# Kernel tuning notes

Hardware: AMD Instinct MI355X
Metric: run time of the kernel (lower is better)

## Reference

```python
import jax, jax.numpy as jnp
import numpy as np
import math

N_HEAD = 8
KERNEL_EPS = 1e-3   # performer-pytorch kernel_epsilon
BN_EPS = 1e-5


def _orthogonal_random_features(m, d, seed=0):
    # gaussian_orthogonal_random_matrix with scaling=0 (performer-pytorch)
    rng = np.random.default_rng(seed)
    blocks = []
    for _ in range(math.ceil(m / d)):
        q, _ = np.linalg.qr(rng.standard_normal((d, d)))
        blocks.append(q.T)
    final = np.concatenate(blocks, axis=0)[:m]
    multiplier = np.linalg.norm(rng.standard_normal((m, d)), axis=1)
    return (multiplier[:, None] * final).astype(np.float32)


def setup_inputs() -> dict:
    key = jax.random.key(0)
    ks = jax.random.split(key, 12)
    B, C, H, W = 16, 256, 56, 56
    d_head = C // N_HEAD                       # 32
    m = int(d_head * math.log(d_head))         # 110 (nb_features default)
    s = 0.02
    inp = {
        "x": jax.random.normal(ks[0], (B, C, H, W), jnp.float32),
        "bn1_gamma": jnp.ones((C,), jnp.float32),
        "bn1_beta": jnp.zeros((C,), jnp.float32),
        "bn2_gamma": jnp.ones((C,), jnp.float32),
        "bn2_beta": jnp.zeros((C,), jnp.float32),
        "Wq": jax.random.normal(ks[1], (C, C), jnp.float32) * s,
        "bq": jnp.zeros((C,), jnp.float32),
        "Wk": jax.random.normal(ks[2], (C, C), jnp.float32) * s,
        "bk": jnp.zeros((C,), jnp.float32),
        "Wv": jax.random.normal(ks[3], (C, C), jnp.float32) * s,
        "bv": jnp.zeros((C,), jnp.float32),
        "Wo": jax.random.normal(ks[4], (C, C), jnp.float32) * s,
        "bo": jnp.zeros((C,), jnp.float32),
        "proj": jnp.asarray(_orthogonal_random_features(m, d_head)),
        "conv_w": jax.random.normal(ks[5], (C, C, 3, 3), jnp.float32) * 0.02,
    }
    return inp


def _batchnorm(x, gamma, beta):
    # training-mode BatchNorm2d: batch statistics over (N, H, W)
    mean = jnp.mean(x, axis=(0, 2, 3), keepdims=True)
    var = jnp.var(x, axis=(0, 2, 3), keepdims=True)
    xn = (x - mean) * jax.lax.rsqrt(var + BN_EPS)
    return gamma[None, :, None, None] * xn + beta[None, :, None, None]


def _performer_attention(x, Wq, bq, Wk, bk, Wv, bv, Wo, bo, proj):
    # x: [B, C, H, W]; flatten spatial dims into a token sequence
    b, c, hh, ww = x.shape
    n = hh * ww
    d = c // N_HEAD
    t = x.reshape(b, c, n).transpose(0, 2, 1)  # [b, n, c]

    def split_heads(z):
        return z.reshape(b, n, N_HEAD, d).transpose(0, 2, 1, 3)  # [b, h, n, d]

    q = split_heads(t @ Wq + bq)
    k = split_heads(t @ Wk + bk)
    v = split_heads(t @ Wv + bv)

    # generalized (ReLU) kernel features, data_normalizer = d**-0.25
    norm = d ** -0.25
    phi_q = jax.nn.relu(jnp.einsum('bhnd,md->bhnm', q * norm, proj)) + KERNEL_EPS
    phi_k = jax.nn.relu(jnp.einsum('bhnd,md->bhnm', k * norm, proj)) + KERNEL_EPS

    # non-causal linear attention: O(n * m * d)
    k_sum = phi_k.sum(axis=2)                                   # [b, h, m]
    d_inv = 1.0 / jnp.einsum('bhnm,bhm->bhn', phi_q, k_sum)     # [b, h, n]
    ctx = jnp.einsum('bhnm,bhnd->bhmd', phi_k, v)               # [b, h, m, d]
    out = jnp.einsum('bhnm,bhmd->bhnd', phi_q, ctx) * d_inv[..., None]

    out = out.transpose(0, 2, 1, 3).reshape(b, n, c)            # merge heads
    out = out @ Wo + bo                                         # to_out (dropout = identity at eval)
    return out.transpose(0, 2, 1).reshape(b, c, hh, ww)


def reference(x, bn1_gamma, bn1_beta, bn2_gamma, bn2_beta,
              Wq, bq, Wk, bk, Wv, bv, Wo, bo, proj, conv_w):
    residual = x
    out = jax.nn.relu(_batchnorm(x, bn1_gamma, bn1_beta))
    out = _performer_attention(out, Wq, bq, Wk, bk, Wv, bv, Wo, bo, proj)
    out = out + x
    out = jax.nn.relu(_batchnorm(out, bn2_gamma, bn2_beta))
    out = jax.lax.conv_general_dilated(
        out, conv_w, window_strides=(1, 1), padding=((1, 1), (1, 1)),
        dimension_numbers=('NCHW', 'OIHW', 'NCHW'))
    return out + residual
```

## Files before the change

kernel.cpp:

```cpp
#include <hip/hip_runtime.h>


typedef short short8 __attribute__((ext_vector_type(8)));
typedef float f32x4 __attribute__((ext_vector_type(4)));

#define DEVI static __device__ __forceinline__

#define CDIM 256
#define SDIM 3136
#define NTOK 50176
#define NHEAD 8
#define DHEAD 32
#define MFEAT 110
#define NORMC 0.42044820762685725f
#define NPIX 50176.0f

DEVI unsigned short f2bf(float f) {
  union { float f; unsigned u; } v; v.f = f;
  unsigned r = v.u + 0x7fffu + ((v.u >> 16) & 1u);
  return (unsigned short)(r >> 16);
}

DEVI float bf2f(short h) {
  union { unsigned u; float f; } v;
  v.u = ((unsigned)(unsigned short)h) << 16;
  return v.f;
}

DEVI f32x4 mfma16(short8 a, short8 b, f32x4 c) {
  return __builtin_amdgcn_mfma_f32_16x16x32_bf16(a, b, c, 0, 0, 0);
}

DEVI unsigned long long pack4(const unsigned short* h) {
  return (unsigned long long)(h[0] | ((unsigned)h[1] << 16)) |
         ((unsigned long long)(h[2] | ((unsigned)h[3] << 16)) << 32);
}

__global__ void zero_kernel(float* p, int n) {
  for (int i = blockIdx.x * blockDim.x + threadIdx.x; i < n; i += gridDim.x * blockDim.x)
    p[i] = 0.f;
}

__global__ void prep_kernel(const float* __restrict__ Wq, const float* __restrict__ Wk,
                            const float* __restrict__ Wv, const float* __restrict__ Wo,
                            const float* __restrict__ proj, const float* __restrict__ conv_w,
                            short* __restrict__ Bqkv, short* __restrict__ WoT,
                            short* __restrict__ Bconv, short* __restrict__ projb) {
  const int t0 = blockIdx.x * blockDim.x + threadIdx.x;
  const int stride = gridDim.x * blockDim.x;
  for (int idx = t0; idx < 3 * 65536; idx += stride) {
    const int sel = idx >> 16, r = idx & 65535;
    const int ks = r >> 13, nf = (r >> 9) & 15, lane = (r >> 3) & 63, j = r & 7;
    const int n = nf * 16 + (lane & 15), k = ks * 32 + (lane >> 4) * 8 + j;
    const float* W = (sel == 0) ? Wq : ((sel == 1) ? Wk : Wv);
    Bqkv[idx] = (short)f2bf(W[k * 256 + n]);
  }
  for (int idx = t0; idx < 65536; idx += stride) {
    const int ks = idx >> 13, nf = (idx >> 9) & 15, lane = (idx >> 3) & 63, j = idx & 7;
    const int n = nf * 16 + (lane & 15), k = ks * 32 + (lane >> 4) * 8 + j;
    WoT[idx] = (short)f2bf(Wo[k * 256 + n]);
  }
  for (int idx = t0; idx < 9 * 65536; idx += stride) {
    const int off = idx >> 16, r = idx & 65535;
    const int ks = r >> 13, nf = (r >> 9) & 15, lane = (r >> 3) & 63, j = r & 7;
    const int oc = nf * 16 + (lane & 15), cin = ks * 32 + (lane >> 4) * 8 + j;
    Bconv[idx] = (short)f2bf(conv_w[(oc * 256 + cin) * 9 + off]);
  }
  for (int idx = t0; idx < 128 * 32; idx += stride) {
    const int row = idx >> 5, kk = idx & 31;
    const float v = (row < MFEAT) ? proj[row * 32 + kk] * NORMC : 0.f;
    projb[idx] = (short)f2bf(v);
  }
}

__global__ void bn_stats_kernel(const float* __restrict__ src, float* __restrict__ sums) {
  const int c = blockIdx.x & 255, b = blockIdx.x >> 8;
  const float* p = src + ((size_t)b * CDIM + c) * SDIM;
  float s = 0.f, s2 = 0.f;
  for (int i = threadIdx.x; i < SDIM; i += 256) {
    const float v = p[i];
    s += v; s2 += v * v;
  }
  for (int o = 32; o > 0; o >>= 1) { s += __shfl_down(s, o); s2 += __shfl_down(s2, o); }
  __shared__ float ls[4], ls2[4];
  const int w = threadIdx.x >> 6;
  if ((threadIdx.x & 63) == 0) { ls[w] = s; ls2[w] = s2; }
  __syncthreads();
  if (threadIdx.x == 0) {
    s = ls[0] + ls[1] + ls[2] + ls[3];
    s2 = ls2[0] + ls2[1] + ls2[2] + ls2[3];
    atomicAdd(&sums[c], s);
    atomicAdd(&sums[256 + c], s2);
  }
}

__global__ void bn_final_kernel(const float* __restrict__ sums, const float* __restrict__ gamma,
                                const float* __restrict__ beta, float* __restrict__ scsh) {
  const int c = threadIdx.x;
  const float mean = sums[c] * (1.f / NPIX);
  const float var = sums[256 + c] * (1.f / NPIX) - mean * mean;
  const float sc = gamma[c] * rsqrtf(var + 1e-5f);
  scsh[c] = sc;
  scsh[256 + c] = beta[c] - mean * sc;
}

__global__ void transpose_x(const float* __restrict__ x, const float* __restrict__ scsh,
                            short* __restrict__ dst, int mode) {
  __shared__ short T[64][72];
  const int t0 = blockIdx.x * 64;
  const int b = t0 / SDIM;
  const int s0 = t0 - b * SDIM;
  const int c0 = blockIdx.y * 64;
  const int tid = threadIdx.x;
  const int tokl = tid & 63, cl = tid >> 6;
  const float* xb = x + ((size_t)b * CDIM + c0) * SDIM + s0;
#pragma unroll
  for (int i = 0; i < 16; ++i) {
    const int c = i * 4 + cl;
    float v = xb[(size_t)c * SDIM + tokl];
    if (mode) v = fmaxf(v * scsh[c0 + c] + scsh[256 + c0 + c], 0.f);
    T[c][tokl] = (short)f2bf(v);
  }
  __syncthreads();
#pragma unroll
  for (int j = 0; j < 2; ++j) {
    const int idx = tid + j * 256;
    const int tk = idx >> 3, ch8 = idx & 7;
    unsigned short h[8];
#pragma unroll
    for (int jj = 0; jj < 8; ++jj) h[jj] = (unsigned short)T[ch8 * 8 + jj][tk];
    unsigned long long* p = (unsigned long long*)&dst[(size_t)(t0 + tk) * 256 + c0 + ch8 * 8];
    p[0] = pack4(h);
    p[1] = pack4(h + 4);
  }
}

__global__ __launch_bounds__(256, 4)
void qkv_gemm(const short* __restrict__ u1, const short* __restrict__ BT,
              const float* __restrict__ bq, const float* __restrict__ bk,
              const float* __restrict__ bv,
              short* __restrict__ qo, short* __restrict__ ko, short* __restrict__ vo) {
  __shared__ short A_s[64 * 256];
  const int tid = threadIdx.x;
  const int mtile = blockIdx.x, sel = blockIdx.y;
  const int token0 = mtile * 64;
  {
    const int trow = tid >> 5, cch = tid & 31;
    const short* src = u1 + (size_t)token0 * 256;
#pragma unroll
    for (int i = 0; i < 8; ++i) {
      const int tok = trow + i * 8;
      const short8 vv = *(const short8*)&src[tok * 256 + cch * 8];
      const int phys = cch ^ (tok & 31);
      *(short8*)&A_s[tok * 256 + phys * 8] = vv;
    }
  }
  __syncthreads();

  const int lane = tid & 63, wv = tid >> 6;
  const int quad = lane >> 4, l15 = lane & 15;
  const f32x4 vzero = {0.f, 0.f, 0.f, 0.f};
  f32x4 acc[4][4];
#pragma unroll
  for (int i = 0; i < 4; ++i)
#pragma unroll
    for (int j = 0; j < 4; ++j) acc[i][j] = vzero;
  const short* Bp = BT + ((size_t)sel << 16);
#pragma unroll
  for (int ks = 0; ks < 8; ++ks) {
    short8 af[4], bfr[4];
#pragma unroll
    for (int rf = 0; rf < 4; ++rf) {
      const int row = rf * 16 + l15;
      const int phys = (ks * 4 + quad) ^ (row & 31);
      af[rf] = *(const short8*)&A_s[row * 256 + phys * 8];
    }
#pragma unroll
    for (int cf = 0; cf < 4; ++cf)
      bfr[cf] = *(const short8*)&Bp[((((ks << 4) | (wv << 2) | cf) << 6) | lane) << 3];
#pragma unroll
    for (int rf = 0; rf < 4; ++rf)
#pragma unroll
      for (int cf = 0; cf < 4; ++cf)
        acc[rf][cf] = mfma16(af[rf], bfr[cf], acc[rf][cf]);
  }

  const int bb = token0 / SDIM;
  const int s0 = token0 - bb * SDIM;
#pragma unroll
  for (int cf = 0; cf < 4; ++cf) {
    const int chn = wv * 64 + cf * 16 + l15;
    const int head = chn >> 5, dd = chn & 31;
    const float bias = (sel == 0) ? bq[chn] : ((sel == 1) ? bk[chn] : bv[chn]);
#pragma unroll
    for (int rf = 0; rf < 4; ++rf) {
      const int ss = s0 + rf * 16 + quad * 4;
      if (sel < 2) {
        short* dst = (sel == 0) ? qo : ko;
        short* p = dst + ((size_t)(bb * NHEAD + head) * SDIM) * DHEAD + dd;
#pragma unroll
        for (int r = 0; r < 4; ++r)
          p[(size_t)(ss + r) * DHEAD] = (short)f2bf(acc[rf][cf][r] + bias);
      } else {
        unsigned short h4[4];
#pragma unroll
        for (int r = 0; r < 4; ++r) h4[r] = f2bf(acc[rf][cf][r] + bias);
        *(unsigned long long*)(vo + ((size_t)(bb * NHEAD + head) * DHEAD + dd) * SDIM + ss) = pack4(h4);
      }
    }
  }
}

__global__ __launch_bounds__(256, 2)
void attn_phase1(const short* __restrict__ kk, const short* __restrict__ vt,
                 const short* __restrict__ projb, float* __restrict__ ctx_acc,
                 float* __restrict__ ksum) {
  __shared__ short proj_s[128 * 40];
  __shared__ short phi_s[4][128 * 40];
  const int tid = threadIdx.x;
  const int bh = blockIdx.x >> 1, halfI = blockIdx.x & 1;
  for (int i = tid; i < 128 * 32; i += 256)
    proj_s[(i >> 5) * 40 + (i & 31)] = projb[i];
  __syncthreads();
  const int lane = tid & 63, wv = tid >> 6;
  const int quad = lane >> 4, l15 = lane & 15;
  const short* kb = kk + (size_t)bh * SDIM * DHEAD;
  const short* vb = vt + (size_t)bh * DHEAD * SDIM;
  short* myphi = phi_s[wv];
  const f32x4 vzero = {0.f, 0.f, 0.f, 0.f};
  f32x4 cacc[8][2];
  float ks_acc[8];
#pragma unroll
  for (int i = 0; i < 8; ++i) { cacc[i][0] = vzero; cacc[i][1] = vzero; ks_acc[i] = 0.f; }

  for (int ch = halfI * 4 + wv; ch < 98; ch += 8) {
    const int tok0 = ch * 32;
    short8 afr[2];
    afr[0] = *(const short8*)&kb[(size_t)(tok0 + l15) * DHEAD + quad * 8];
    afr[1] = *(const short8*)&kb[(size_t)(tok0 + 16 + l15) * DHEAD + quad * 8];
#pragma unroll
    for (int cf = 0; cf < 8; ++cf) {
      const short8 bfr = *(const short8*)&proj_s[(cf * 16 + l15) * 40 + quad * 8];
      const float epsv = (cf < 6) ? 1e-3f : ((cf == 6) ? ((l15 < 14) ? 1e-3f : 0.f) : 0.f);
#pragma unroll
      for (int fr = 0; fr < 2; ++fr) {
        f32x4 p = mfma16(afr[fr], bfr, vzero);
        unsigned short h4[4];
        float srow = 0.f;
#pragma unroll
        for (int r = 0; r < 4; ++r) {
          const float pv = fmaxf(p[r], 0.f) + epsv;
          srow += pv;
          h4[r] = f2bf(pv);
        }
        ks_acc[cf] += srow;
        *(unsigned long long*)&myphi[(cf * 16 + l15) * 40 + fr * 16 + quad * 4] = pack4(h4);
      }
    }
    short8 bv2[2];
    bv2[0] = *(const short8*)&vb[(size_t)l15 * SDIM + tok0 + quad * 8];
    bv2[1] = *(const short8*)&vb[(size_t)(16 + l15) * SDIM + tok0 + quad * 8];
#pragma unroll
    for (int mfr = 0; mfr < 8; ++mfr) {
      const short8 a2 = *(const short8*)&myphi[(mfr * 16 + l15) * 40 + quad * 8];
      cacc[mfr][0] = mfma16(a2, bv2[0], cacc[mfr][0]);
      cacc[mfr][1] = mfma16(a2, bv2[1], cacc[mfr][1]);
    }
  }
#pragma unroll
  for (int cf = 0; cf < 8; ++cf) {
    float v = ks_acc[cf];
    v += __shfl_xor(v, 16);
    v += __shfl_xor(v, 32);
    if (lane < 16) atomicAdd(&ksum[bh * 128 + cf * 16 + lane], v);
  }
  float* cb = ctx_acc + (size_t)bh * 4096;
#pragma unroll
  for (int mfr = 0; mfr < 8; ++mfr)
#pragma unroll
    for (int df = 0; df < 2; ++df)
#pragma unroll
      for (int r = 0; r < 4; ++r)
        atomicAdd(&cb[(mfr * 16 + quad * 4 + r) * 32 + df * 16 + l15], cacc[mfr][df][r]);
}

__global__ __launch_bounds__(256, 2)
void attn_phase2(const short* __restrict__ qq, const float* __restrict__ ctx_acc,
                 const float* __restrict__ ksum, const short* __restrict__ projb,
                 short* __restrict__ Yn) {
  __shared__ short proj_s[128 * 40];
  __shared__ short ctx_s[48 * 136];
  __shared__ short phi_s[4][32 * 136];
  const int tid = threadIdx.x;
  const int bh = blockIdx.x >> 1, halfI = blockIdx.x & 1;
  for (int i = tid; i < 128 * 32; i += 256)
    proj_s[(i >> 5) * 40 + (i & 31)] = projb[i];
  {
    const float* ca = ctx_acc + (size_t)bh * 4096;
    const float* ks = ksum + bh * 128;
    for (int i = tid; i < 48 * 128; i += 256) {
      const int row = i >> 7, mf = i & 127;
      const float v = (row < 32) ? ca[mf * 32 + row] : ((row == 32) ? ks[mf] : 0.f);
      ctx_s[row * 136 + mf] = (short)f2bf(v);
    }
  }
  __syncthreads();
  const int lane = tid & 63, wv = tid >> 6;
  const int quad = lane >> 4, l15 = lane & 15;
  const int b = bh >> 3, head = bh & 7;
  const short* qb = qq + (size_t)bh * SDIM * DHEAD;
  short* myphi = phi_s[wv];
  const f32x4 vzero = {0.f, 0.f, 0.f, 0.f};

  for (int ch = halfI * 4 + wv; ch < 98; ch += 8) {
    const int tok0 = ch * 32;
    short8 afr[2];
    afr[0] = *(const short8*)&qb[(size_t)(tok0 + l15) * DHEAD + quad * 8];
    afr[1] = *(const short8*)&qb[(size_t)(tok0 + 16 + l15) * DHEAD + quad * 8];
#pragma unroll
    for (int cf = 0; cf < 8; ++cf) {
      const short8 bfr = *(const short8*)&proj_s[(cf * 16 + l15) * 40 + quad * 8];
      const float epsv = (cf < 6) ? 1e-3f : ((cf == 6) ? ((l15 < 14) ? 1e-3f : 0.f) : 0.f);
#pragma unroll
      for (int fr = 0; fr < 2; ++fr) {
        f32x4 p = mfma16(afr[fr], bfr, vzero);
#pragma unroll
        for (int r = 0; r < 4; ++r) {
          const float pv = fmaxf(p[r], 0.f) + epsv;
          myphi[(fr * 16 + quad * 4 + r) * 136 + cf * 16 + l15] = (short)f2bf(pv);
        }
      }
    }
    f32x4 oacc[2][3];
#pragma unroll
    for (int fr = 0; fr < 2; ++fr)
#pragma unroll
      for (int c3 = 0; c3 < 3; ++c3) oacc[fr][c3] = vzero;
#pragma unroll
    for (int ksI = 0; ksI < 4; ++ksI) {
      short8 a3[2];
      a3[0] = *(const short8*)&myphi[l15 * 136 + ksI * 32 + quad * 8];
      a3[1] = *(const short8*)&myphi[(16 + l15) * 136 + ksI * 32 + quad * 8];
#pragma unroll
      for (int c3 = 0; c3 < 3; ++c3) {
        const short8 b3 = *(const short8*)&ctx_s[(c3 * 16 + l15) * 136 + ksI * 32 + quad * 8];
        oacc[0][c3] = mfma16(a3[0], b3, oacc[0][c3]);
        oacc[1][c3] = mfma16(a3[1], b3, oacc[1][c3]);
      }
    }
#pragma unroll
    for (int fr = 0; fr < 2; ++fr) {
      float dinv[4];
#pragma unroll
      for (int r = 0; r < 4; ++r) {
        const float den = __shfl(oacc[fr][2][r], quad << 4);
        dinv[r] = 1.f / den;
      }
#pragma unroll
      for (int c3 = 0; c3 < 2; ++c3)
#pragma unroll
        for (int r = 0; r < 4; ++r)
          myphi[(fr * 16 + quad * 4 + r) * 40 + c3 * 16 + l15] =
              (short)f2bf(oacc[fr][c3][r] * dinv[r]);
    }
    const size_t trow0 = (size_t)(b * SDIM + tok0) * 256 + head * 32;
#pragma unroll
    for (int it = 0; it < 2; ++it) {
      const int idx = it * 64 + lane;
      const int tl = idx >> 2, c4 = idx & 3;
      const short8 vv = *(const short8*)&myphi[tl * 40 + c4 * 8];
      *(short8*)&Yn[trow0 + (size_t)tl * 256 + c4 * 8] = vv;
    }
  }
}

__global__ __launch_bounds__(256, 4)
void wo_gemm(const short* __restrict__ Yn, const short* __restrict__ WoT,
             const float* __restrict__ bo, const short* __restrict__ xh,
             short* __restrict__ z, float* __restrict__ sums) {
  __shared__ short A_s[64 * 264];
  const int tid = threadIdx.x;
  const int mtile = blockIdx.x;
  const int token0 = mtile * 64;
  {
    const int trow = tid >> 5, cch = tid & 31;
    const short* src = Yn + (size_t)token0 * 256;
#pragma unroll
    for (int i = 0; i < 8; ++i) {
      const int tok = trow + i * 8;
      const short8 vv = *(const short8*)&src[tok * 256 + cch * 8];
      const int phys = cch ^ (tok & 31);
      *(short8*)&A_s[tok * 256 + phys * 8] = vv;
    }
  }
  __syncthreads();

  const int lane = tid & 63, wv = tid >> 6;
  const int quad = lane >> 4, l15 = lane & 15;
  const f32x4 vzero = {0.f, 0.f, 0.f, 0.f};
  f32x4 acc[4][4];
#pragma unroll
  for (int i = 0; i < 4; ++i)
#pragma unroll
    for (int j = 0; j < 4; ++j) acc[i][j] = vzero;
#pragma unroll
  for (int ks = 0; ks < 8; ++ks) {
    short8 af[4], bfr[4];
#pragma unroll
    for (int rf = 0; rf < 4; ++rf) {
      const int row = rf * 16 + l15;
      const int phys = (ks * 4 + quad) ^ (row & 31);
      af[rf] = *(const short8*)&A_s[row * 256 + phys * 8];
    }
#pragma unroll
    for (int cf = 0; cf < 4; ++cf)
      bfr[cf] = *(const short8*)&WoT[((((ks << 4) | (wv << 2) | cf) << 6) | lane) << 3];
#pragma unroll
    for (int rf = 0; rf < 4; ++rf)
#pragma unroll
      for (int cf = 0; cf < 4; ++cf)
        acc[rf][cf] = mfma16(af[rf], bfr[cf], acc[rf][cf]);
  }
  __syncthreads();
  short* zt = A_s;
#pragma unroll
  for (int cf = 0; cf < 4; ++cf) {
    const int ocl = wv * 64 + cf * 16 + l15;
    const float bias = bo[ocl];
#pragma unroll
    for (int rf = 0; rf < 4; ++rf) {
      const int tl = rf * 16 + quad * 4;
#pragma unroll
      for (int r = 0; r < 4; ++r)
        zt[(tl + r) * 264 + ocl] = (short)f2bf(acc[rf][cf][r] + bias);
    }
  }
  __syncthreads();
  float s[8], s2[8];
#pragma unroll
  for (int j = 0; j < 8; ++j) { s[j] = 0.f; s2[j] = 0.f; }
#pragma unroll
  for (int j = 0; j < 8; ++j) {
    const int idx = tid + j * 256;
    const int tl = idx >> 5, ch = idx & 31;
    const short8 zv = *(const short8*)&zt[tl * 264 + ch * 8];
    const size_t gbase = (size_t)(token0 + tl) * 256 + ch * 8;
    const short8 xv = *(const short8*)&xh[gbase];
    unsigned short h[8];
#pragma unroll
    for (int jj = 0; jj < 8; ++jj) {
      h[jj] = f2bf(bf2f(zv[jj]) + bf2f(xv[jj]));
      const float f = bf2f((short)h[jj]);
      s[jj] += f; s2[jj] += f * f;
    }
    unsigned long long* p = (unsigned long long*)&z[gbase];
    p[0] = pack4(h);
    p[1] = pack4(h + 4);
  }
  __syncthreads();
  float* L = (float*)A_s;
#pragma unroll
  for (int j = 0; j < 8; ++j) { L[tid * 16 + j] = s[j]; L[tid * 16 + 8 + j] = s2[j]; }
  __syncthreads();
  const int c = tid, cgi = c >> 3, j2 = c & 7;
  float a = 0.f, b2 = 0.f;
#pragma unroll
  for (int tr = 0; tr < 8; ++tr) {
    a += L[(tr * 32 + cgi) * 16 + j2];
    b2 += L[(tr * 32 + cgi) * 16 + 8 + j2];
  }
  atomicAdd(&sums[c], a);
  atomicAdd(&sums[256 + c], b2);
}

__global__ __launch_bounds__(256, 4)
void conv_gemm(const short* __restrict__ zin, const float* __restrict__ scsh,
               const short* __restrict__ Bc, const float* __restrict__ x,
               float* __restrict__ out) {
  __shared__ short A_s[40 * 256];
  const int tid = threadIdx.x;
  const int bid = blockIdx.x;
  const int mtile = (bid & 7) * 196 + (bid >> 3);
  const int bb = mtile / 98, s0 = (mtile - bb * 98) * 32;
  const short* ub = zin + (size_t)bb * SDIM * 256;
  const int lane = tid & 63, wv = tid >> 6;
  const int quad = lane >> 4, l15 = lane & 15;
  const f32x4 vzero = {0.f, 0.f, 0.f, 0.f};
  const short8 szero = {0, 0, 0, 0, 0, 0, 0, 0};
  f32x4 acc[2][4];
#pragma unroll
  for (int i = 0; i < 2; ++i)
#pragma unroll
    for (int j = 0; j < 4; ++j) acc[i][j] = vzero;

  const int cch = tid & 31;
  float sc_r[8], sh_r[8];
#pragma unroll
  for (int j = 0; j < 8; ++j) {
    sc_r[j] = scsh[cch * 8 + j];
    sh_r[j] = scsh[256 + cch * 8 + j];
  }

  int vy[2], vx[2];
#pragma unroll
  for (int rf = 0; rf < 2; ++rf) {
    const int so = s0 + rf * 16 + l15;
    vy[rf] = so / 56;
    vx[rf] = so - vy[rf] * 56;
  }

  short8 pref[5];
#define LOAD_DY(DYI)                                                           \
  {                                                                            \
    const int srow0 = s0 + ((DYI)-1) * 56 - 1;                                 \
    _Pragma("unroll") for (int it = 0; it < 5; ++it) {                         \
      const int chunk = tid + it * 256;                                        \
      const int idx = chunk >> 5;                                              \
      const int s = srow0 + idx;                                               \
      short8 vv = {0, 0, 0, 0, 0, 0, 0, 0};                                    \
      if ((unsigned)s < (unsigned)SDIM) {                                      \
        const short8 raw = *(const short8*)&ub[(size_t)s * 256 + cch * 8];     \
        unsigned short hh[8];                                                  \
        _Pragma("unroll") for (int jj = 0; jj < 8; ++jj)                       \
            hh[jj] = f2bf(fmaxf(bf2f(raw[jj]) * sc_r[jj] + sh_r[jj], 0.f));    \
        _Pragma("unroll") for (int jj = 0; jj < 8; ++jj)                       \
            vv[jj] = (short)hh[jj];                                            \
      }                                                                        \
      pref[it] = vv;                                                           \
    }                                                                          \
  }

  LOAD_DY(0);
#pragma unroll
  for (int dyi = 0; dyi < 3; ++dyi) {
    if (dyi) __syncthreads();
#pragma unroll
    for (int it = 0; it < 5; ++it) {
      const int chunk = tid + it * 256;
      const int idx = chunk >> 5;
      const int phys = cch ^ (idx & 31);
      *(short8*)&A_s[idx * 256 + phys * 8] = pref[it];
    }
    __syncthreads();
    if (dyi < 2) LOAD_DY(dyi + 1);
#pragma unroll
    for (int dxi = 0; dxi < 3; ++dxi) {
      const short* Bp = Bc + ((dyi * 3 + dxi) << 16);
      bool vmask[2];
#pragma unroll
      for (int rf = 0; rf < 2; ++rf)
        vmask[rf] = ((unsigned)(vy[rf] + dyi - 1) < 56u) &&
                    ((unsigned)(vx[rf] + dxi - 1) < 56u);
#pragma unroll
      for (int ks = 0; ks < 8; ++ks) {
        short8 af[2], bfr[4];
#pragma unroll
        for (int rf = 0; rf < 2; ++rf) {
          const int row = rf * 16 + l15 + dxi;
          const int phys = (ks * 4 + quad) ^ (row & 31);
          const short8 a = *(const short8*)&A_s[row * 256 + phys * 8];
          af[rf] = vmask[rf] ? a : szero;
        }
#pragma unroll
        for (int cf = 0; cf < 4; ++cf)
          bfr[cf] = *(const short8*)&Bp[((((ks << 4) | (wv << 2) | cf) << 6) | lane) << 3];
#pragma unroll
        for (int rf = 0; rf < 2; ++rf)
#pragma unroll
          for (int cf = 0; cf < 4; ++cf)
            acc[rf][cf] = mfma16(af[rf], bfr[cf], acc[rf][cf]);
      }
    }
  }
#undef LOAD_DY

#pragma unroll
  for (int cf = 0; cf < 4; ++cf) {
    const int oc = wv * 64 + cf * 16 + l15;
#pragma unroll
    for (int rf = 0; rf < 2; ++rf) {
      const int ss = s0 + rf * 16 + quad * 4;
      const size_t base = ((size_t)(bb * CDIM + oc)) * SDIM + ss;
      const f32x4 xv = *(const f32x4*)(x + base);
      f32x4 res;
#pragma unroll
      for (int r = 0; r < 4; ++r) res[r] = acc[rf][cf][r] + xv[r];
      *(f32x4*)(out + base) = res;
    }
  }
}

extern "C" void kernel_launch(void* const* d_in, const int* in_sizes, int n_in,
                              void* d_out, int out_size, void* d_ws, size_t ws_size,
                              hipStream_t stream) {
  const float* x      = (const float*)d_in[0];
  const float* bn1_g  = (const float*)d_in[1];
  const float* bn1_b  = (const float*)d_in[2];
  const float* bn2_g  = (const float*)d_in[3];
  const float* bn2_b  = (const float*)d_in[4];
  const float* Wq     = (const float*)d_in[5];
  const float* bq     = (const float*)d_in[6];
  const float* Wk     = (const float*)d_in[7];
  const float* bk     = (const float*)d_in[8];
  const float* Wv     = (const float*)d_in[9];
  const float* bv     = (const float*)d_in[10];
  const float* Wo     = (const float*)d_in[11];
  const float* bo     = (const float*)d_in[12];
  const float* proj   = (const float*)d_in[13];
  const float* conv_w = (const float*)d_in[14];
  float* out = (float*)d_out;
  char* ws = (char*)d_ws;

  const size_t OFF_K     = 0;
  const size_t OFF_V     = 25690112;
  const size_t OFF_BQKV  = 51380224;
  const size_t OFF_WOT   = 51773440;
  const size_t OFF_BCONV = 51904512;
  const size_t OFF_PROJB = 53084160;
  const size_t OFF_CTXA  = 53092352;
  const size_t OFF_KSUM  = 55189504;
  const size_t OFF_BN1S  = 55255040;
  const size_t OFF_BN2S  = 55257088;
  const size_t OFF_SC1   = 55259136;
  const size_t OFF_SC2   = 55261184;
  const size_t WS_NEEDED = 56836096;

  if (ws_size < WS_NEEDED) {
    zero_kernel<<<2048, 256, 0, stream>>>(out, out_size);
    return;
  }

  short* qb    = (short*)d_out;
  short* half2 = (short*)d_out + 12845056;
  short* kb    = (short*)(ws + OFF_K);
  short* vtb   = (short*)(ws + OFF_V);
  short* Yn    = (short*)(ws + OFF_K);
  short* zbuf  = (short*)(ws + OFF_V);
  short* Bqkv  = (short*)(ws + OFF_BQKV);
  short* WoT   = (short*)(ws + OFF_WOT);
  short* Bconv = (short*)(ws + OFF_BCONV);
  short* projb = (short*)(ws + OFF_PROJB);
  float* ctxa  = (float*)(ws + OFF_CTXA);
  float* ksum  = (float*)(ws + OFF_KSUM);
  float* bn1s  = (float*)(ws + OFF_BN1S);
  float* bn2s  = (float*)(ws + OFF_BN2S);
  float* sc1   = (float*)(ws + OFF_SC1);
  float* sc2   = (float*)(ws + OFF_SC2);

  zero_kernel<<<512, 256, 0, stream>>>(ctxa, (2097152 + 65536 + 2048 + 2048) / 4);
  prep_kernel<<<256, 256, 0, stream>>>(Wq, Wk, Wv, Wo, proj, conv_w, Bqkv, WoT, Bconv, projb);
  bn_stats_kernel<<<4096, 256, 0, stream>>>(x, bn1s);
  bn_final_kernel<<<1, 256, 0, stream>>>(bn1s, bn1_g, bn1_b, sc1);
  transpose_x<<<dim3(784, 4), 256, 0, stream>>>(x, sc1, half2, 1);
  qkv_gemm<<<dim3(784, 3), 256, 0, stream>>>(half2, Bqkv, bq, bk, bv, qb, kb, vtb);
  attn_phase1<<<256, 256, 0, stream>>>(kb, vtb, projb, ctxa, ksum);
  attn_phase2<<<256, 256, 0, stream>>>(qb, ctxa, ksum, projb, Yn);
  transpose_x<<<dim3(784, 4), 256, 0, stream>>>(x, sc1, half2, 0);
  wo_gemm<<<784, 256, 0, stream>>>(Yn, WoT, bo, half2, zbuf, bn2s);
  bn_final_kernel<<<1, 256, 0, stream>>>(bn2s, bn2_g, bn2_b, sc2);
  conv_gemm<<<1568, 256, 0, stream>>>(zbuf, sc2, Bconv, x, out);
}
```

Measured before the change: 516.6 us.

## Fuse residual into Wo epilogue, merge QKV passes, precompute BN2-ReLU tensor

The second transpose of x is removed: the Wo GEMM epilogue now reads fp32 x directly and adds the residual before rounding to bf16. The QKV GEMM loops over the three weight matrices inside one block, so the A tile is staged once instead of three times. BN2 plus ReLU is moved out of the conv prefetch into a separate elementwise kernel that writes a normalized bf16 buffer. This removes the ninefold redundant normalization in conv_gemm at the cost of an extra full-tensor read and write. attn_phase1 launch bounds are also raised to 3 blocks per CU.

Result: slower. 839.2 us (+62.4%).

```diff
diff --git a/kernel.cpp b/kernel.cpp
--- a/kernel.cpp
+++ b/kernel.cpp
@@ -105,7 +105,7 @@
 }
 
 __global__ void transpose_x(const float* __restrict__ x, const float* __restrict__ scsh,
-                            short* __restrict__ dst, int mode) {
+                            short* __restrict__ dst) {
   __shared__ short T[64][72];
   const int t0 = blockIdx.x * 64;
   const int b = t0 / SDIM;
@@ -118,7 +118,7 @@
   for (int i = 0; i < 16; ++i) {
     const int c = i * 4 + cl;
     float v = xb[(size_t)c * SDIM + tokl];
-    if (mode) v = fmaxf(v * scsh[c0 + c] + scsh[256 + c0 + c], 0.f);
+    v = fmaxf(v * scsh[c0 + c] + scsh[256 + c0 + c], 0.f);
     T[c][tokl] = (short)f2bf(v);
   }
   __syncthreads();
@@ -130,6 +130,25 @@
 #pragma unroll
     for (int jj = 0; jj < 8; ++jj) h[jj] = (unsigned short)T[ch8 * 8 + jj][tk];
     unsigned long long* p = (unsigned long long*)&dst[(size_t)(t0 + tk) * 256 + c0 + ch8 * 8];
+    p[0] = pack4(h);
+    p[1] = pack4(h + 4);
+  }
+}
+
+__global__ void u2_kernel(const short* __restrict__ z, const float* __restrict__ scsh,
+                          short* __restrict__ u2) {
+  const int nchunks = NTOK * 32;
+  for (int idx = blockIdx.x * blockDim.x + threadIdx.x; idx < nchunks;
+       idx += gridDim.x * blockDim.x) {
+    const int cch = idx & 31;
+    const short8 v = *(const short8*)&z[(size_t)idx * 8];
+    unsigned short h[8];
+#pragma unroll
+    for (int j = 0; j < 8; ++j) {
+      const int c = cch * 8 + j;
+      h[j] = f2bf(fmaxf(bf2f(v[j]) * scsh[c] + scsh[256 + c], 0.f));
+    }
+    unsigned long long* p = (unsigned long long*)&u2[(size_t)idx * 8];
     p[0] = pack4(h);
     p[1] = pack4(h + 4);
   }
@@ -142,7 +161,7 @@
               short* __restrict__ qo, short* __restrict__ ko, short* __restrict__ vo) {
   __shared__ short A_s[64 * 256];
   const int tid = threadIdx.x;
-  const int mtile = blockIdx.x, sel = blockIdx.y;
+  const int mtile = blockIdx.x;
   const int token0 = mtile * 64;
   {
     const int trow = tid >> 5, cch = tid & 31;
@@ -160,58 +179,61 @@
   const int lane = tid & 63, wv = tid >> 6;
   const int quad = lane >> 4, l15 = lane & 15;
   const f32x4 vzero = {0.f, 0.f, 0.f, 0.f};
-  f32x4 acc[4][4];
-#pragma unroll
-  for (int i = 0; i < 4; ++i)
-#pragma unroll
-    for (int j = 0; j < 4; ++j) acc[i][j] = vzero;
-  const short* Bp = BT + ((size_t)sel << 16);
-#pragma unroll
-  for (int ks = 0; ks < 8; ++ks) {
-    short8 af[4], bfr[4];
-#pragma unroll
-    for (int rf = 0; rf < 4; ++rf) {
-      const int row = rf * 16 + l15;
-      const int phys = (ks * 4 + quad) ^ (row & 31);
-      af[rf] = *(const short8*)&A_s[row * 256 + phys * 8];
-    }
-#pragma unroll
-    for (int cf = 0; cf < 4; ++cf)
-      bfr[cf] = *(const short8*)&Bp[((((ks << 4) | (wv << 2) | cf) << 6) | lane) << 3];
-#pragma unroll
-    for (int rf = 0; rf < 4; ++rf)
-#pragma unroll
-      for (int cf = 0; cf < 4; ++cf)
-        acc[rf][cf] = mfma16(af[rf], bfr[cf], acc[rf][cf]);
-  }
-
   const int bb = token0 / SDIM;
   const int s0 = token0 - bb * SDIM;
-#pragma unroll
-  for (int cf = 0; cf < 4; ++cf) {
-    const int chn = wv * 64 + cf * 16 + l15;
-    const int head = chn >> 5, dd = chn & 31;
-    const float bias = (sel == 0) ? bq[chn] : ((sel == 1) ? bk[chn] : bv[chn]);
-#pragma unroll
-    for (int rf = 0; rf < 4; ++rf) {
-      const int ss = s0 + rf * 16 + quad * 4;
-      if (sel < 2) {
-        short* dst = (sel == 0) ? qo : ko;
-        short* p = dst + ((size_t)(bb * NHEAD + head) * SDIM) * DHEAD + dd;
-#pragma unroll
-        for (int r = 0; r < 4; ++r)
-          p[(size_t)(ss + r) * DHEAD] = (short)f2bf(acc[rf][cf][r] + bias);
-      } else {
-        unsigned short h4[4];
-#pragma unroll
-        for (int r = 0; r < 4; ++r) h4[r] = f2bf(acc[rf][cf][r] + bias);
-        *(unsigned long long*)(vo + ((size_t)(bb * NHEAD + head) * DHEAD + dd) * SDIM + ss) = pack4(h4);
+
+  for (int sel = 0; sel < 3; ++sel) {
+    f32x4 acc[4][4];
+#pragma unroll
+    for (int i = 0; i < 4; ++i)
+#pragma unroll
+      for (int j = 0; j < 4; ++j) acc[i][j] = vzero;
+    const short* Bp = BT + ((size_t)sel << 16);
+#pragma unroll
+    for (int ks = 0; ks < 8; ++ks) {
+      short8 af[4], bfr[4];
+#pragma unroll
+      for (int rf = 0; rf < 4; ++rf) {
+        const int row = rf * 16 + l15;
+        const int phys = (ks * 4 + quad) ^ (row & 31);
+        af[rf] = *(const short8*)&A_s[row * 256 + phys * 8];
       }
-    }
-  }
-}
-
-__global__ __launch_bounds__(256, 2)
+#pragma unroll
+      for (int cf = 0; cf < 4; ++cf)
+        bfr[cf] = *(const short8*)&Bp[((((ks << 4) | (wv << 2) | cf) << 6) | lane) << 3];
+#pragma unroll
+      for (int rf = 0; rf < 4; ++rf)
+#pragma unroll
+        for (int cf = 0; cf < 4; ++cf)
+          acc[rf][cf] = mfma16(af[rf], bfr[cf], acc[rf][cf]);
+    }
+
+#pragma unroll
+    for (int cf = 0; cf < 4; ++cf) {
+      const int chn = wv * 64 + cf * 16 + l15;
+      const int head = chn >> 5, dd = chn & 31;
+      const float bias = (sel == 0) ? bq[chn] : ((sel == 1) ? bk[chn] : bv[chn]);
+#pragma unroll
+      for (int rf = 0; rf < 4; ++rf) {
+        const int ss = s0 + rf * 16 + quad * 4;
+        if (sel < 2) {
+          short* dst = (sel == 0) ? qo : ko;
+          short* p = dst + ((size_t)(bb * NHEAD + head) * SDIM) * DHEAD + dd;
+#pragma unroll
+          for (int r = 0; r < 4; ++r)
+            p[(size_t)(ss + r) * DHEAD] = (short)f2bf(acc[rf][cf][r] + bias);
+        } else {
+          unsigned short h4[4];
+#pragma unroll
+          for (int r = 0; r < 4; ++r) h4[r] = f2bf(acc[rf][cf][r] + bias);
+          *(unsigned long long*)(vo + ((size_t)(bb * NHEAD + head) * DHEAD + dd) * SDIM + ss) = pack4(h4);
+        }
+      }
+    }
+  }
+}
+
+__global__ __launch_bounds__(256, 3)
 void attn_phase1(const short* __restrict__ kk, const short* __restrict__ vt,
                  const short* __restrict__ projb, float* __restrict__ ctx_acc,
                  float* __restrict__ ksum) {
@@ -376,7 +398,7 @@
 
 __global__ __launch_bounds__(256, 4)
 void wo_gemm(const short* __restrict__ Yn, const short* __restrict__ WoT,
-             const float* __restrict__ bo, const short* __restrict__ xh,
+             const float* __restrict__ bo, const float* __restrict__ x,
              short* __restrict__ z, float* __restrict__ sums) {
   __shared__ short A_s[64 * 264];
   const int tid = threadIdx.x;
@@ -421,6 +443,8 @@
       for (int cf = 0; cf < 4; ++cf)
         acc[rf][cf] = mfma16(af[rf], bfr[cf], acc[rf][cf]);
   }
+  const int bb = token0 / SDIM;
+  const int s0 = token0 - bb * SDIM;
   __syncthreads();
   short* zt = A_s;
 #pragma unroll
@@ -430,9 +454,10 @@
 #pragma unroll
     for (int rf = 0; rf < 4; ++rf) {
       const int tl = rf * 16 + quad * 4;
+      const f32x4 xv = *(const f32x4*)(x + ((size_t)(bb * CDIM + ocl)) * SDIM + s0 + tl);
 #pragma unroll
       for (int r = 0; r < 4; ++r)
-        zt[(tl + r) * 264 + ocl] = (short)f2bf(acc[rf][cf][r] + bias);
+        zt[(tl + r) * 264 + ocl] = (short)f2bf(acc[rf][cf][r] + bias + xv[r]);
     }
   }
   __syncthreads();
@@ -444,18 +469,12 @@
     const int idx = tid + j * 256;
     const int tl = idx >> 5, ch = idx & 31;
     const short8 zv = *(const short8*)&zt[tl * 264 + ch * 8];
-    const size_t gbase = (size_t)(token0 + tl) * 256 + ch * 8;
-    const short8 xv = *(const short8*)&xh[gbase];
-    unsigned short h[8];
 #pragma unroll
     for (int jj = 0; jj < 8; ++jj) {
-      h[jj] = f2bf(bf2f(zv[jj]) + bf2f(xv[jj]));
-      const float f = bf2f((short)h[jj]);
+      const float f = bf2f(zv[jj]);
       s[jj] += f; s2[jj] += f * f;
     }
-    unsigned long long* p = (unsigned long long*)&z[gbase];
-    p[0] = pack4(h);
-    p[1] = pack4(h + 4);
+    *(short8*)&z[(size_t)(token0 + tl) * 256 + ch * 8] = zv;
   }
   __syncthreads();
   float* L = (float*)A_s;
@@ -474,15 +493,14 @@
 }
 
 __global__ __launch_bounds__(256, 4)
-void conv_gemm(const short* __restrict__ zin, const float* __restrict__ scsh,
-               const short* __restrict__ Bc, const float* __restrict__ x,
-               float* __restrict__ out) {
+void conv_gemm(const short* __restrict__ u2, const short* __restrict__ Bc,
+               const float* __restrict__ x, float* __restrict__ out) {
   __shared__ short A_s[40 * 256];
   const int tid = threadIdx.x;
   const int bid = blockIdx.x;
   const int mtile = (bid & 7) * 196 + (bid >> 3);
   const int bb = mtile / 98, s0 = (mtile - bb * 98) * 32;
-  const short* ub = zin + (size_t)bb * SDIM * 256;
+  const short* ub = u2 + (size_t)bb * SDIM * 256;
   const int lane = tid & 63, wv = tid >> 6;
   const int quad = lane >> 4, l15 = lane & 15;
   const f32x4 vzero = {0.f, 0.f, 0.f, 0.f};
@@ -492,14 +510,6 @@
   for (int i = 0; i < 2; ++i)
 #pragma unroll
     for (int j = 0; j < 4; ++j) acc[i][j] = vzero;
-
-  const int cch = tid & 31;
-  float sc_r[8], sh_r[8];
-#pragma unroll
-  for (int j = 0; j < 8; ++j) {
-    sc_r[j] = scsh[cch * 8 + j];
-    sh_r[j] = scsh[256 + cch * 8 + j];
-  }
 
   int vy[2], vx[2];
 #pragma unroll
@@ -515,17 +525,11 @@
     const int srow0 = s0 + ((DYI)-1) * 56 - 1;                                 \
     _Pragma("unroll") for (int it = 0; it < 5; ++it) {                         \
       const int chunk = tid + it * 256;                                        \
-      const int idx = chunk >> 5;                                              \
+      const int idx = chunk >> 5, cchl = chunk & 31;                           \
       const int s = srow0 + idx;                                               \
       short8 vv = {0, 0, 0, 0, 0, 0, 0, 0};                                    \
-      if ((unsigned)s < (unsigned)SDIM) {                                      \
-        const short8 raw = *(const short8*)&ub[(size_t)s * 256 + cch * 8];     \
-        unsigned short hh[8];                                                  \
-        _Pragma("unroll") for (int jj = 0; jj < 8; ++jj)                       \
-            hh[jj] = f2bf(fmaxf(bf2f(raw[jj]) * sc_r[jj] + sh_r[jj], 0.f));    \
-        _Pragma("unroll") for (int jj = 0; jj < 8; ++jj)                       \
-            vv[jj] = (short)hh[jj];                                            \
-      }                                                                        \
+      if ((unsigned)s < (unsigned)SDIM)                                        \
+        vv = *(const short8*)&ub[(size_t)s * 256 + cchl * 8];                  \
       pref[it] = vv;                                                           \
     }                                                                          \
   }
@@ -537,8 +541,8 @@
 #pragma unroll
     for (int it = 0; it < 5; ++it) {
       const int chunk = tid + it * 256;
-      const int idx = chunk >> 5;
-      const int phys = cch ^ (idx & 31);
+      const int idx = chunk >> 5, cchl = chunk & 31;
+      const int phys = cchl ^ (idx & 31);
       *(short8*)&A_s[idx * 256 + phys * 8] = pref[it];
     }
     __syncthreads();
@@ -631,11 +635,12 @@
   }
 
   short* qb    = (short*)d_out;
-  short* half2 = (short*)d_out + 12845056;
+  short* u1b   = (short*)d_out + 12845056;
   short* kb    = (short*)(ws + OFF_K);
   short* vtb   = (short*)(ws + OFF_V);
   short* Yn    = (short*)(ws + OFF_K);
   short* zbuf  = (short*)(ws + OFF_V);
+  short* u2b   = (short*)(ws + OFF_K);
   short* Bqkv  = (short*)(ws + OFF_BQKV);
   short* WoT   = (short*)(ws + OFF_WOT);
   short* Bconv = (short*)(ws + OFF_BCONV);
@@ -651,12 +656,12 @@
   prep_kernel<<<256, 256, 0, stream>>>(Wq, Wk, Wv, Wo, proj, conv_w, Bqkv, WoT, Bconv, projb);
   bn_stats_kernel<<<4096, 256, 0, stream>>>(x, bn1s);
   bn_final_kernel<<<1, 256, 0, stream>>>(bn1s, bn1_g, bn1_b, sc1);
-  transpose_x<<<dim3(784, 4), 256, 0, stream>>>(x, sc1, half2, 1);
-  qkv_gemm<<<dim3(784, 3), 256, 0, stream>>>(half2, Bqkv, bq, bk, bv, qb, kb, vtb);
+  transpose_x<<<dim3(784, 4), 256, 0, stream>>>(x, sc1, u1b);
+  qkv_gemm<<<784, 256, 0, stream>>>(u1b, Bqkv, bq, bk, bv, qb, kb, vtb);
   attn_phase1<<<256, 256, 0, stream>>>(kb, vtb, projb, ctxa, ksum);
   attn_phase2<<<256, 256, 0, stream>>>(qb, ctxa, ksum, projb, Yn);
-  transpose_x<<<dim3(784, 4), 256, 0, stream>>>(x, sc1, half2, 0);
-  wo_gemm<<<784, 256, 0, stream>>>(Yn, WoT, bo, half2, zbuf, bn2s);
+  wo_gemm<<<784, 256, 0, stream>>>(Yn, WoT, bo, x, zbuf, bn2s);
   bn_final_kernel<<<1, 256, 0, stream>>>(bn2s, bn2_g, bn2_b, sc2);
-  conv_gemm<<<1568, 256, 0, stream>>>(zbuf, sc2, Bconv, x, out);
-}
+  u2_kernel<<<1024, 256, 0, stream>>>(zbuf, sc2, u2b);
+  conv_gemm<<<1568, 256, 0, stream>>>(u2b, Bconv, x, out);
+}
```
